# Performance work log

Hardware: AMD Instinct MI355X
Metric: run time of the kernel (lower is better)

The kernel has to match this reference:

```python
import jax, jax.numpy as jnp
import numpy as np

INF = 1e9
EPS = 1e-10
LN_EPS = 1e-5
H, CH = 8, 16  # no_heads, c_hidden


def setup_inputs() -> dict:
    key = jax.random.key(0)
    ks = jax.random.split(key, 8)
    B, S, R, C = 1, 2048, 512, 64  # batch, n_seq, n_res, c_in
    sc = 0.02
    m = jax.random.normal(ks[0], (B, S, R, C), jnp.float32)
    mask = jnp.ones((B, S, R), jnp.float32)
    ln_w = jnp.ones((C,), jnp.float32)
    ln_b = jnp.zeros((C,), jnp.float32)
    Wq = jax.random.normal(ks[1], (C, H * CH), jnp.float32) * sc
    Wk = jax.random.normal(ks[2], (C, CH), jnp.float32) * sc
    Wv = jax.random.normal(ks[3], (C, CH), jnp.float32) * sc
    Wg = jax.random.normal(ks[4], (C, H * CH), jnp.float32) * sc
    bg = jnp.ones((H * CH,), jnp.float32)  # gating init: bias = 1
    Wo = jax.random.normal(ks[5], (H * CH, C), jnp.float32) * sc
    bo = jnp.zeros((C,), jnp.float32)
    return {"m": m, "mask": mask, "ln_w": ln_w, "ln_b": ln_b, "Wq": Wq,
            "Wk": Wk, "Wv": Wv, "Wg": Wg, "bg": bg, "Wo": Wo, "bo": bo}


def reference(m, mask, ln_w, ln_b, Wq, Wk, Wv, Wg, bg, Wo, bo):
    # m: [B, S, R, C], mask: [B, S, R]
    m = jnp.swapaxes(m, -2, -3)        # [B, R, S, C] -- attend over seq per column
    mask = jnp.swapaxes(mask, -1, -2)  # [B, R, S]
    # LayerNorm over c_in
    mu = jnp.mean(m, axis=-1, keepdims=True)
    var = jnp.var(m, axis=-1, keepdims=True)
    mn = (m - mu) / jnp.sqrt(var + LN_EPS) * ln_w + ln_b  # [B, R, S, C]
    # masked mean-pooled query over seq dim
    q = jnp.sum(mn * mask[..., None], axis=-2) / (jnp.sum(mask, axis=-1)[..., None] + EPS)  # [B, R, C]
    q = (q @ Wq) * (CH ** -0.5)
    q = q.reshape(*q.shape[:-1], H, CH)  # [B, R, H, CH]
    k = mn @ Wk  # [B, R, S, CH]  (single shared K/V head)
    v = mn @ Wv  # [B, R, S, CH]
    a = jnp.einsum('brhc,brsc->brhs', q, k)
    a = a + (INF * (mask - 1.0))[..., None, :]  # additive mask bias
    a = jax.nn.softmax(a, axis=-1)               # [B, R, H, S]
    o = jnp.einsum('brhs,brsc->brhc', a, v)      # [B, R, H, CH]
    g = jax.nn.sigmoid(mn @ Wg + bg)             # [B, R, S, H*CH]
    g = g.reshape(*g.shape[:-1], H, CH)          # [B, R, S, H, CH]
    o = o[..., None, :, :] * g                   # broadcast pooled attn over seq
    o = o.reshape(*o.shape[:-2], -1)             # [B, R, S, H*CH]
    out = o @ Wo + bo                            # [B, R, S, C]
    return jnp.swapaxes(out, -2, -3)             # [B, S, R, C]
```

## Files before the change

### kernel.cpp

```cpp
#include <hip/hip_runtime.h>
#include <stdint.h>

#define S_ 2048
#define R_ 512
#define C_ 64

typedef unsigned short u16;
typedef __attribute__((ext_vector_type(8))) short bf8_t;
typedef __attribute__((ext_vector_type(4))) float f4_t;

__device__ __forceinline__ u16 f2b(float f) {
    union { float f; unsigned int i; } x; x.f = f;
    unsigned int r = x.i + 0x7fffu + ((x.i >> 16) & 1u);
    return (u16)(r >> 16);
}
__device__ __forceinline__ unsigned int pack2(float a, float b) {
    return (unsigned int)f2b(a) | ((unsigned int)f2b(b) << 16);
}
__device__ __forceinline__ void u4_to_f8(uint4 p, float* f) {
    union { unsigned int i; float f; } x;
    x.i = p.x << 16;         f[0] = x.f;
    x.i = p.x & 0xffff0000u; f[1] = x.f;
    x.i = p.y << 16;         f[2] = x.f;
    x.i = p.y & 0xffff0000u; f[3] = x.f;
    x.i = p.z << 16;         f[4] = x.f;
    x.i = p.z & 0xffff0000u; f[5] = x.f;
    x.i = p.w << 16;         f[6] = x.f;
    x.i = p.w & 0xffff0000u; f[7] = x.f;
}

__global__ __launch_bounds__(256) void k0(
    const float* __restrict__ Wk, const float* __restrict__ Wv,
    const float* __restrict__ Wg, const float* __restrict__ Wo,
    u16* __restrict__ kvT, u16* __restrict__ WgT, u16* __restrict__ WoT)
{
    int i = blockIdx.x * 256 + threadIdx.x;
    if (i < 2048) {
        int j = i >> 6, c = i & 63;
        float w = (j < 16) ? Wk[c * 16 + j] : Wv[c * 16 + (j - 16)];
        kvT[i] = f2b(w);
    }
    {
        int hc = i >> 6, c = i & 63;
        WgT[i] = f2b(Wg[c * 128 + hc]);
    }
    {
        int c = i >> 7, hc = i & 127;
        WoT[i] = f2b(Wo[hc * 64 + c]);
    }
}

__global__ __launch_bounds__(256) void k1a(
    const float* __restrict__ m, const float* __restrict__ mask,
    const float* __restrict__ lnw_g, const float* __restrict__ lnb_g,
    const u16* __restrict__ kvT_g,
    u16* __restrict__ kbuf, u16* __restrict__ vbuf,
    float* __restrict__ qsum, float* __restrict__ msum,
    u16* __restrict__ mns_g)
{
    __shared__ __attribute__((aligned(16))) u16 mns[32 * 72];
    __shared__ __attribute__((aligned(16))) u16 kva[32 * 40];
    __shared__ float qred[4][64];
    __shared__ float msred[4];

    const int tid = threadIdx.x;
    const int bi  = blockIdx.x;
    const int r   = bi >> 6;
    const int s0  = (bi & 63) << 5;
    const int wv = tid >> 6, lane = tid & 63;
    const int r16 = lane & 15, quad = lane >> 4;
    const int mt = wv & 1, nt = wv >> 1;

    bf8_t b0 = *(const bf8_t*)&kvT_g[(nt * 16 + r16) * 64 + quad * 8];
    bf8_t b1 = *(const bf8_t*)&kvT_g[(nt * 16 + r16) * 64 + 32 + quad * 8];

    const int g = tid >> 4, l = tid & 15;
    const float4 lw4 = *(const float4*)&lnw_g[4 * l];
    const float4 lb4 = *(const float4*)&lnb_g[4 * l];

    float4 qacc = {0.f, 0.f, 0.f, 0.f};
    float msacc = 0.f;
    #pragma unroll
    for (int tt = 0; tt < 2; ++tt) {
        int t = g + tt * 16;
        int s = s0 + t;
        size_t base = ((size_t)s * R_ + r) * C_;
        float4 x = *(const float4*)&m[base + 4 * l];
        float sum = x.x + x.y + x.z + x.w;
        float ssq = x.x * x.x + x.y * x.y + x.z * x.z + x.w * x.w;
        #pragma unroll
        for (int off = 1; off <= 8; off <<= 1) {
            sum += __shfl_xor(sum, off);
            ssq += __shfl_xor(ssq, off);
        }
        float mu  = sum * (1.f / 64.f);
        float var = ssq * (1.f / 64.f) - mu * mu;
        float rs  = rsqrtf(var + 1e-5f);
        float4 mn;
        mn.x = (x.x - mu) * rs * lw4.x + lb4.x;
        mn.y = (x.y - mu) * rs * lw4.y + lb4.y;
        mn.z = (x.z - mu) * rs * lw4.z + lb4.z;
        mn.w = (x.w - mu) * rs * lw4.w + lb4.w;
        float mk = mask[(size_t)s * R_ + r];
        qacc.x += mn.x * mk; qacc.y += mn.y * mk;
        qacc.z += mn.z * mk; qacc.w += mn.w * mk;
        if (l == 0) msacc += mk;
        uint2 p; p.x = pack2(mn.x, mn.y); p.y = pack2(mn.z, mn.w);
        *(uint2*)&mns[t * 72 + 4 * l] = p;
        if (mns_g)
            *(uint2*)&mns_g[((size_t)r * S_ + s) * C_ + 4 * l] = p;
    }
    qacc.x += __shfl_xor(qacc.x, 16); qacc.y += __shfl_xor(qacc.y, 16);
    qacc.z += __shfl_xor(qacc.z, 16); qacc.w += __shfl_xor(qacc.w, 16);
    qacc.x += __shfl_xor(qacc.x, 32); qacc.y += __shfl_xor(qacc.y, 32);
    qacc.z += __shfl_xor(qacc.z, 32); qacc.w += __shfl_xor(qacc.w, 32);
    msacc += __shfl_xor(msacc, 16);  msacc += __shfl_xor(msacc, 32);
    if (lane < 16) *(float4*)&qred[wv][4 * lane] = qacc;
    if (lane == 0) msred[wv] = msacc;
    __syncthreads();

    {
        f4_t acc = {0.f, 0.f, 0.f, 0.f};
        bf8_t a0 = *(const bf8_t*)&mns[(mt * 16 + r16) * 72 + quad * 8];
        bf8_t a1 = *(const bf8_t*)&mns[(mt * 16 + r16) * 72 + 32 + quad * 8];
        acc = __builtin_amdgcn_mfma_f32_16x16x32_bf16(a0, b0, acc, 0, 0, 0);
        acc = __builtin_amdgcn_mfma_f32_16x16x32_bf16(a1, b1, acc, 0, 0, 0);
        #pragma unroll
        for (int i = 0; i < 4; ++i) {
            int row = mt * 16 + quad * 4 + i;
            kva[row * 40 + nt * 16 + r16] = f2b(acc[i]);
        }
    }
    __syncthreads();

    for (int uidx = tid; uidx < 512; uidx += 256) {
        int t = uidx >> 4, u = uidx & 15;
        unsigned int val = *(const unsigned int*)&kva[t * 40 + u * 2];
        int s = s0 + t;
        size_t tb = ((size_t)r * S_ + s) * 16;
        if (u < 8) *(unsigned int*)&kbuf[tb + u * 2] = val;
        else       *(unsigned int*)&vbuf[tb + (u - 8) * 2] = val;
    }
    if (tid < 64) {
        float tot = qred[0][tid] + qred[1][tid] + qred[2][tid] + qred[3][tid];
        atomicAdd(&qsum[r * 64 + tid], tot);
    }
    if (tid == 0) atomicAdd(&msum[r], msred[0] + msred[1] + msred[2] + msred[3]);
}

__global__ __launch_bounds__(256) void k1b(
    const float* __restrict__ qsum, const float* __restrict__ msum,
    const float* __restrict__ Wq, const float* __restrict__ mask,
    const u16* __restrict__ kbuf, const u16* __restrict__ vbuf,
    float* __restrict__ opool)
{
    __shared__ float qbar[64];
    __shared__ float qh[128];
    const int tid = threadIdx.x;
    const int r   = blockIdx.x;

    if (tid < 64) qbar[tid] = qsum[r * 64 + tid] / (msum[r] + 1e-10f);
    __syncthreads();
    if (tid < 128) {
        float a = 0.f;
        #pragma unroll 8
        for (int c = 0; c < 64; ++c) a += qbar[c] * Wq[c * 128 + tid];
        qh[tid] = a * 0.25f;
    }
    __syncthreads();

    const int wv = tid >> 6, lane = tid & 63;
    const int h0 = wv, h1 = wv + 4;
    float qa[16], qb[16];
    #pragma unroll
    for (int ch = 0; ch < 16; ++ch) { qa[ch] = qh[h0 * 16 + ch]; qb[ch] = qh[h1 * 16 + ch]; }

    float m0 = -1e30f, m1 = -1e30f;
    for (int i = 0; i < 32; ++i) {
        int s = i * 64 + lane;
        size_t tb = ((size_t)r * S_ + s) * 16;
        float kf[16];
        u4_to_f8(*(const uint4*)&kbuf[tb], kf);
        u4_to_f8(*(const uint4*)&kbuf[tb + 8], kf + 8);
        float bias = (mask[(size_t)s * R_ + r] - 1.f) * 1e9f;
        float a0 = bias, a1 = bias;
        #pragma unroll
        for (int ch = 0; ch < 16; ++ch) { a0 += qa[ch] * kf[ch]; a1 += qb[ch] * kf[ch]; }
        m0 = fmaxf(m0, a0); m1 = fmaxf(m1, a1);
    }
    #pragma unroll
    for (int off = 1; off < 64; off <<= 1) {
        m0 = fmaxf(m0, __shfl_xor(m0, off));
        m1 = fmaxf(m1, __shfl_xor(m1, off));
    }
    float l0 = 0.f, l1 = 0.f;
    float o0[16], o1[16];
    #pragma unroll
    for (int ch = 0; ch < 16; ++ch) { o0[ch] = 0.f; o1[ch] = 0.f; }
    for (int i = 0; i < 32; ++i) {
        int s = i * 64 + lane;
        size_t tb = ((size_t)r * S_ + s) * 16;
        float kf[16], vf[16];
        u4_to_f8(*(const uint4*)&kbuf[tb], kf);
        u4_to_f8(*(const uint4*)&kbuf[tb + 8], kf + 8);
        u4_to_f8(*(const uint4*)&vbuf[tb], vf);
        u4_to_f8(*(const uint4*)&vbuf[tb + 8], vf + 8);
        float bias = (mask[(size_t)s * R_ + r] - 1.f) * 1e9f;
        float a0 = bias, a1 = bias;
        #pragma unroll
        for (int ch = 0; ch < 16; ++ch) { a0 += qa[ch] * kf[ch]; a1 += qb[ch] * kf[ch]; }
        float w0 = expf(a0 - m0), w1 = expf(a1 - m1);
        l0 += w0; l1 += w1;
        #pragma unroll
        for (int ch = 0; ch < 16; ++ch) { o0[ch] += w0 * vf[ch]; o1[ch] += w1 * vf[ch]; }
    }
    #pragma unroll
    for (int off = 1; off < 64; off <<= 1) {
        l0 += __shfl_xor(l0, off); l1 += __shfl_xor(l1, off);
        #pragma unroll
        for (int ch = 0; ch < 16; ++ch) {
            o0[ch] += __shfl_xor(o0[ch], off);
            o1[ch] += __shfl_xor(o1[ch], off);
        }
    }
    if (lane == 0) {
        float inv0 = 1.f / l0, inv1 = 1.f / l1;
        #pragma unroll
        for (int ch = 0; ch < 16; ++ch) {
            opool[r * 128 + h0 * 16 + ch] = o0[ch] * inv0;
            opool[r * 128 + h1 * 16 + ch] = o1[ch] * inv1;
        }
    }
}

__global__ __launch_bounds__(256) void k2m(
    const u16* __restrict__ mns_g,
    const u16* __restrict__ WgT_g, const u16* __restrict__ WoT_g,
    const float* __restrict__ bg, const float* __restrict__ bo,
    const float* __restrict__ opool, float* __restrict__ out)
{
    __shared__ __attribute__((aligned(16))) u16 olds[32 * 136];
    __shared__ __attribute__((aligned(16))) float outs[32 * 68];
    __shared__ float opl[128], bgl[128];
    __shared__ float bol[64];

    const int tid = threadIdx.x;
    const int bi  = blockIdx.x;
    const int r   = bi >> 6;
    const int s0  = (bi & 63) << 5;
    const int wv = tid >> 6, lane = tid & 63;
    const int r16 = lane & 15, quad = lane >> 4;

    const int mt  = wv >> 1;
    const int nb2 = (wv & 1) * 4;
    const int nb3 = (wv & 1) * 2;

    bf8_t wg[4][2], wo[2][4];
    #pragma unroll
    for (int i = 0; i < 4; ++i)
        #pragma unroll
        for (int kt = 0; kt < 2; ++kt)
            wg[i][kt] = *(const bf8_t*)&WgT_g[((nb2 + i) * 16 + r16) * 64 + kt * 32 + quad * 8];
    #pragma unroll
    for (int i = 0; i < 2; ++i)
        #pragma unroll
        for (int kt = 0; kt < 4; ++kt)
            wo[i][kt] = *(const bf8_t*)&WoT_g[((nb3 + i) * 16 + r16) * 128 + kt * 32 + quad * 8];

    size_t abase = ((size_t)r * S_ + s0 + mt * 16 + r16) * C_;
    bf8_t a0 = *(const bf8_t*)&mns_g[abase + quad * 8];
    bf8_t a1 = *(const bf8_t*)&mns_g[abase + 32 + quad * 8];

    if (tid < 128) { opl[tid] = opool[r * 128 + tid]; bgl[tid] = bg[tid]; }
    if (tid < 64)  { bol[tid] = bo[tid]; }
    __syncthreads();

    #pragma unroll
    for (int i = 0; i < 4; ++i) {
        f4_t acc = {0.f, 0.f, 0.f, 0.f};
        acc = __builtin_amdgcn_mfma_f32_16x16x32_bf16(a0, wg[i][0], acc, 0, 0, 0);
        acc = __builtin_amdgcn_mfma_f32_16x16x32_bf16(a1, wg[i][1], acc, 0, 0, 0);
        int hc = (nb2 + i) * 16 + r16;
        float og = opl[hc], bgv = bgl[hc];
        #pragma unroll
        for (int ii = 0; ii < 4; ++ii) {
            int row = mt * 16 + quad * 4 + ii;
            float z  = acc[ii] + bgv;
            float gv = 1.f / (1.f + expf(-z));
            olds[row * 136 + hc] = f2b(og * gv);
        }
    }
    __syncthreads();

    #pragma unroll
    for (int i = 0; i < 2; ++i) {
        f4_t acc = {0.f, 0.f, 0.f, 0.f};
        #pragma unroll
        for (int kt = 0; kt < 4; ++kt) {
            bf8_t a = *(const bf8_t*)&olds[(mt * 16 + r16) * 136 + kt * 32 + quad * 8];
            acc = __builtin_amdgcn_mfma_f32_16x16x32_bf16(a, wo[i][kt], acc, 0, 0, 0);
        }
        int c = (nb3 + i) * 16 + r16;
        float bov = bol[c];
        #pragma unroll
        for (int ii = 0; ii < 4; ++ii) {
            int row = mt * 16 + quad * 4 + ii;
            outs[row * 68 + c] = acc[ii] + bov;
        }
    }
    __syncthreads();

    const int g = tid >> 4, l = tid & 15;
    #pragma unroll
    for (int tt = 0; tt < 2; ++tt) {
        int t = g + tt * 16;
        int s = s0 + t;
        size_t base = ((size_t)s * R_ + r) * C_;
        *(float4*)&out[base + 4 * l] = *(const float4*)&outs[t * 68 + 4 * l];
    }
}

__global__ __launch_bounds__(256) void k2f(
    const float* __restrict__ m,
    const float* __restrict__ lnw_g, const float* __restrict__ lnb_g,
    const u16* __restrict__ WgT_g, const u16* __restrict__ WoT_g,
    const float* __restrict__ bg, const float* __restrict__ bo,
    const float* __restrict__ opool, float* __restrict__ out)
{
    __shared__ __attribute__((aligned(16))) u16 mns[32 * 72];
    __shared__ __attribute__((aligned(16))) u16 olds[32 * 136];
    __shared__ __attribute__((aligned(16))) float outs[32 * 68];
    __shared__ float opl[128], bgl[128];
    __shared__ float bol[64];

    const int tid = threadIdx.x;
    const int bi  = blockIdx.x;
    const int r   = bi >> 6;
    const int s0  = (bi & 63) << 5;
    const int wv = tid >> 6, lane = tid & 63;
    const int r16 = lane & 15, quad = lane >> 4;
    const int mt  = wv >> 1;
    const int nb2 = (wv & 1) * 4;
    const int nb3 = (wv & 1) * 2;

    bf8_t wg[4][2], wo[2][4];
    #pragma unroll
    for (int i = 0; i < 4; ++i)
        #pragma unroll
        for (int kt = 0; kt < 2; ++kt)
            wg[i][kt] = *(const bf8_t*)&WgT_g[((nb2 + i) * 16 + r16) * 64 + kt * 32 + quad * 8];
    #pragma unroll
    for (int i = 0; i < 2; ++i)
        #pragma unroll
        for (int kt = 0; kt < 4; ++kt)
            wo[i][kt] = *(const bf8_t*)&WoT_g[((nb3 + i) * 16 + r16) * 128 + kt * 32 + quad * 8];

    if (tid < 128) { opl[tid] = opool[r * 128 + tid]; bgl[tid] = bg[tid]; }
    if (tid < 64)  { bol[tid] = bo[tid]; }

    const int g = tid >> 4, l = tid & 15;
    const float4 lw4 = *(const float4*)&lnw_g[4 * l];
    const float4 lb4 = *(const float4*)&lnb_g[4 * l];
    #pragma unroll
    for (int tt = 0; tt < 2; ++tt) {
        int t = g + tt * 16;
        int s = s0 + t;
        size_t base = ((size_t)s * R_ + r) * C_;
        float4 x = *(const float4*)&m[base + 4 * l];
        float sum = x.x + x.y + x.z + x.w;
        float ssq = x.x * x.x + x.y * x.y + x.z * x.z + x.w * x.w;
        #pragma unroll
        for (int off = 1; off <= 8; off <<= 1) {
            sum += __shfl_xor(sum, off);
            ssq += __shfl_xor(ssq, off);
        }
        float mu  = sum * (1.f / 64.f);
        float var = ssq * (1.f / 64.f) - mu * mu;
        float rs  = rsqrtf(var + 1e-5f);
        uint2 p;
        p.x = pack2((x.x - mu) * rs * lw4.x + lb4.x, (x.y - mu) * rs * lw4.y + lb4.y);
        p.y = pack2((x.z - mu) * rs * lw4.z + lb4.z, (x.w - mu) * rs * lw4.w + lb4.w);
        *(uint2*)&mns[t * 72 + 4 * l] = p;
    }
    __syncthreads();

    #pragma unroll
    for (int i = 0; i < 4; ++i) {
        f4_t acc = {0.f, 0.f, 0.f, 0.f};
        #pragma unroll
        for (int kt = 0; kt < 2; ++kt) {
            bf8_t a = *(const bf8_t*)&mns[(mt * 16 + r16) * 72 + kt * 32 + quad * 8];
            acc = __builtin_amdgcn_mfma_f32_16x16x32_bf16(a, wg[i][kt], acc, 0, 0, 0);
        }
        int hc = (nb2 + i) * 16 + r16;
        float og = opl[hc], bgv = bgl[hc];
        #pragma unroll
        for (int ii = 0; ii < 4; ++ii) {
            int row = mt * 16 + quad * 4 + ii;
            float z  = acc[ii] + bgv;
            float gv = 1.f / (1.f + expf(-z));
            olds[row * 136 + hc] = f2b(og * gv);
        }
    }
    __syncthreads();

    #pragma unroll
    for (int i = 0; i < 2; ++i) {
        f4_t acc = {0.f, 0.f, 0.f, 0.f};
        #pragma unroll
        for (int kt = 0; kt < 4; ++kt) {
            bf8_t a = *(const bf8_t*)&olds[(mt * 16 + r16) * 136 + kt * 32 + quad * 8];
            acc = __builtin_amdgcn_mfma_f32_16x16x32_bf16(a, wo[i][kt], acc, 0, 0, 0);
        }
        int c = (nb3 + i) * 16 + r16;
        float bov = bol[c];
        #pragma unroll
        for (int ii = 0; ii < 4; ++ii) {
            int row = mt * 16 + quad * 4 + ii;
            outs[row * 68 + c] = acc[ii] + bov;
        }
    }
    __syncthreads();

    #pragma unroll
    for (int tt = 0; tt < 2; ++tt) {
        int t = g + tt * 16;
        int s = s0 + t;
        size_t base = ((size_t)s * R_ + r) * C_;
        *(float4*)&out[base + 4 * l] = *(const float4*)&outs[t * 68 + 4 * l];
    }
}

extern "C" void kernel_launch(void* const* d_in, const int* in_sizes, int n_in,
                              void* d_out, int out_size, void* d_ws, size_t ws_size,
                              hipStream_t stream)
{
    const float* m    = (const float*)d_in[0];
    const float* mask = (const float*)d_in[1];
    const float* lnw  = (const float*)d_in[2];
    const float* lnb  = (const float*)d_in[3];
    const float* Wq   = (const float*)d_in[4];
    const float* Wk   = (const float*)d_in[5];
    const float* Wv   = (const float*)d_in[6];
    const float* Wg   = (const float*)d_in[7];
    const float* bg   = (const float*)d_in[8];
    const float* Wo   = (const float*)d_in[9];
    const float* bo   = (const float*)d_in[10];
    float* out = (float*)d_out;

    char* ws = (char*)d_ws;
    u16*   kbuf  = (u16*)ws;
    u16*   vbuf  = (u16*)(ws + 33554432ull);
    float* qsum  = (float*)(ws + 67108864ull);
    float* msum  = (float*)(ws + 67239936ull);
    float* opool = (float*)(ws + 67241984ull);
    u16*   kvT   = (u16*)(ws + 67504128ull);
    u16*   WgT   = (u16*)(ws + 67508224ull);
    u16*   WoT   = (u16*)(ws + 67524608ull);
    u16*   mns_g = (u16*)(ws + 67540992ull);
    const size_t WS_NEED_MNS = 67540992ull + 134217728ull;
    const bool use_mns = ws_size >= WS_NEED_MNS;

    hipMemsetAsync(ws + 67108864ull, 0, 131072 + 2048, stream);
    k0<<<32, 256, 0, stream>>>(Wk, Wv, Wg, Wo, kvT, WgT, WoT);
    k1a<<<32768, 256, 0, stream>>>(m, mask, lnw, lnb, kvT, kbuf, vbuf, qsum, msum,
                                   use_mns ? mns_g : (u16*)nullptr);
    k1b<<<512, 256, 0, stream>>>(qsum, msum, Wq, mask, kbuf, vbuf, opool);
    if (use_mns)
        k2m<<<32768, 256, 0, stream>>>(mns_g, WgT, WoT, bg, bo, opool, out);
    else
        k2f<<<32768, 256, 0, stream>>>(m, lnw, lnb, WgT, WoT, bg, bo, opool, out);
}
```

Baseline: 849.2 us.

## Split pooled attention over sequence chunks with a separate combine kernel

The per-column attention kernel, which previously used 512 blocks each looping over all 2048 sequence positions, is split into 4096 blocks that each handle a 256-position chunk. Each block writes its partial max, sum and weighted V to a workspace buffer, and a small combine kernel merges the eight chunks per column with a log-sum-exp rescale. This is meant to fill the GPU better during that phase. Separately, expf and the division in the sigmoid gate are replaced with the fast __expf and rcp intrinsics, trading a little accuracy for cheaper transcendentals. The chunked path runs only when the workspace is large enough, and it adds a kernel launch and an extra round trip through global memory for the partial results.

```diff
diff --git a/kernel.cpp b/kernel.cpp
--- a/kernel.cpp
+++ b/kernel.cpp
@@ -148,7 +148,120 @@
     if (tid == 0) atomicAdd(&msum[r], msred[0] + msred[1] + msred[2] + msred[3]);
 }
 
-__global__ __launch_bounds__(256) void k1b(
+__global__ __launch_bounds__(256) void k1bp(
+    const float* __restrict__ qsum, const float* __restrict__ msum,
+    const float* __restrict__ Wq, const float* __restrict__ mask,
+    const u16* __restrict__ kbuf, const u16* __restrict__ vbuf,
+    float* __restrict__ pbuf)
+{
+    __shared__ float qbar[64];
+    __shared__ float qh[128];
+    const int tid = threadIdx.x;
+    const int bi  = blockIdx.x;
+    const int r   = bi >> 3;
+    const int ck  = bi & 7;
+
+    if (tid < 64) qbar[tid] = qsum[r * 64 + tid] / (msum[r] + 1e-10f);
+    __syncthreads();
+    if (tid < 128) {
+        float a = 0.f;
+        #pragma unroll 8
+        for (int c = 0; c < 64; ++c) a += qbar[c] * Wq[c * 128 + tid];
+        qh[tid] = a * 0.25f;
+    }
+    __syncthreads();
+
+    const int wv = tid >> 6, lane = tid & 63;
+    const int h0 = wv, h1 = wv + 4;
+    float qa[16], qb[16];
+    #pragma unroll
+    for (int ch = 0; ch < 16; ++ch) { qa[ch] = qh[h0 * 16 + ch]; qb[ch] = qh[h1 * 16 + ch]; }
+
+    const int sbase = ck * 256;
+    float m0 = -1e30f, m1 = -1e30f;
+    #pragma unroll
+    for (int i = 0; i < 4; ++i) {
+        int s = sbase + i * 64 + lane;
+        size_t tb = ((size_t)r * S_ + s) * 16;
+        float kf[16];
+        u4_to_f8(*(const uint4*)&kbuf[tb], kf);
+        u4_to_f8(*(const uint4*)&kbuf[tb + 8], kf + 8);
+        float bias = (mask[(size_t)s * R_ + r] - 1.f) * 1e9f;
+        float a0 = bias, a1 = bias;
+        #pragma unroll
+        for (int ch = 0; ch < 16; ++ch) { a0 += qa[ch] * kf[ch]; a1 += qb[ch] * kf[ch]; }
+        m0 = fmaxf(m0, a0); m1 = fmaxf(m1, a1);
+    }
+    #pragma unroll
+    for (int off = 1; off < 64; off <<= 1) {
+        m0 = fmaxf(m0, __shfl_xor(m0, off));
+        m1 = fmaxf(m1, __shfl_xor(m1, off));
+    }
+    float l0 = 0.f, l1 = 0.f;
+    float o0[16], o1[16];
+    #pragma unroll
+    for (int ch = 0; ch < 16; ++ch) { o0[ch] = 0.f; o1[ch] = 0.f; }
+    #pragma unroll
+    for (int i = 0; i < 4; ++i) {
+        int s = sbase + i * 64 + lane;
+        size_t tb = ((size_t)r * S_ + s) * 16;
+        float kf[16], vf[16];
+        u4_to_f8(*(const uint4*)&kbuf[tb], kf);
+        u4_to_f8(*(const uint4*)&kbuf[tb + 8], kf + 8);
+        u4_to_f8(*(const uint4*)&vbuf[tb], vf);
+        u4_to_f8(*(const uint4*)&vbuf[tb + 8], vf + 8);
+        float bias = (mask[(size_t)s * R_ + r] - 1.f) * 1e9f;
+        float a0 = bias, a1 = bias;
+        #pragma unroll
+        for (int ch = 0; ch < 16; ++ch) { a0 += qa[ch] * kf[ch]; a1 += qb[ch] * kf[ch]; }
+        float w0 = __expf(a0 - m0), w1 = __expf(a1 - m1);
+        l0 += w0; l1 += w1;
+        #pragma unroll
+        for (int ch = 0; ch < 16; ++ch) { o0[ch] += w0 * vf[ch]; o1[ch] += w1 * vf[ch]; }
+    }
+    #pragma unroll
+    for (int off = 1; off < 64; off <<= 1) {
+        l0 += __shfl_xor(l0, off); l1 += __shfl_xor(l1, off);
+        #pragma unroll
+        for (int ch = 0; ch < 16; ++ch) {
+            o0[ch] += __shfl_xor(o0[ch], off);
+            o1[ch] += __shfl_xor(o1[ch], off);
+        }
+    }
+    if (lane == 0) {
+        size_t p0 = (((size_t)r * 8 + h0) * 8 + ck) * 18;
+        size_t p1 = (((size_t)r * 8 + h1) * 8 + ck) * 18;
+        pbuf[p0] = m0; pbuf[p0 + 1] = l0;
+        pbuf[p1] = m1; pbuf[p1 + 1] = l1;
+        #pragma unroll
+        for (int ch = 0; ch < 16; ++ch) {
+            pbuf[p0 + 2 + ch] = o0[ch];
+            pbuf[p1 + 2 + ch] = o1[ch];
+        }
+    }
+}
+
+__global__ __launch_bounds__(128) void k1c(
+    const float* __restrict__ pbuf, float* __restrict__ opool)
+{
+    const int r = blockIdx.x;
+    const int tid = threadIdx.x;
+    const int h = tid >> 4, ch = tid & 15;
+    size_t base = (((size_t)r * 8 + h) * 8) * 18;
+    float M = -1e30f;
+    #pragma unroll
+    for (int i = 0; i < 8; ++i) M = fmaxf(M, pbuf[base + i * 18]);
+    float L = 0.f, O = 0.f;
+    #pragma unroll
+    for (int i = 0; i < 8; ++i) {
+        float sc = __expf(pbuf[base + i * 18] - M);
+        L += pbuf[base + i * 18 + 1] * sc;
+        O += pbuf[base + i * 18 + 2 + ch] * sc;
+    }
+    opool[r * 128 + tid] = O / L;
+}
+
+__global__ __launch_bounds__(256) void k1b_mono(
     const float* __restrict__ qsum, const float* __restrict__ msum,
     const float* __restrict__ Wq, const float* __restrict__ mask,
     const u16* __restrict__ kbuf, const u16* __restrict__ vbuf,
@@ -209,7 +322,7 @@
         float a0 = bias, a1 = bias;
         #pragma unroll
         for (int ch = 0; ch < 16; ++ch) { a0 += qa[ch] * kf[ch]; a1 += qb[ch] * kf[ch]; }
-        float w0 = expf(a0 - m0), w1 = expf(a1 - m1);
+        float w0 = __expf(a0 - m0), w1 = __expf(a1 - m1);
         l0 += w0; l1 += w1;
         #pragma unroll
         for (int ch = 0; ch < 16; ++ch) { o0[ch] += w0 * vf[ch]; o1[ch] += w1 * vf[ch]; }
@@ -286,7 +399,7 @@
         for (int ii = 0; ii < 4; ++ii) {
             int row = mt * 16 + quad * 4 + ii;
             float z  = acc[ii] + bgv;
-            float gv = 1.f / (1.f + expf(-z));
+            float gv = __builtin_amdgcn_rcpf(1.f + __expf(-z));
             olds[row * 136 + hc] = f2b(og * gv);
         }
     }
@@ -398,7 +511,7 @@
         for (int ii = 0; ii < 4; ++ii) {
             int row = mt * 16 + quad * 4 + ii;
             float z  = acc[ii] + bgv;
-            float gv = 1.f / (1.f + expf(-z));
+            float gv = __builtin_amdgcn_rcpf(1.f + __expf(-z));
             olds[row * 136 + hc] = f2b(og * gv);
         }
     }
@@ -458,14 +571,22 @@
     u16*   WgT   = (u16*)(ws + 67508224ull);
     u16*   WoT   = (u16*)(ws + 67524608ull);
     u16*   mns_g = (u16*)(ws + 67540992ull);
-    const size_t WS_NEED_MNS = 67540992ull + 134217728ull;
-    const bool use_mns = ws_size >= WS_NEED_MNS;
+    float* pbuf  = (float*)(ws + 201758720ull);
+    const size_t NEED_MNS = 67540992ull + 134217728ull;
+    const size_t NEED_PB  = 201758720ull + 2359296ull;
+    const bool use_mns = ws_size >= NEED_MNS;
+    const bool use_pb  = ws_size >= NEED_PB;
 
     hipMemsetAsync(ws + 67108864ull, 0, 131072 + 2048, stream);
     k0<<<32, 256, 0, stream>>>(Wk, Wv, Wg, Wo, kvT, WgT, WoT);
     k1a<<<32768, 256, 0, stream>>>(m, mask, lnw, lnb, kvT, kbuf, vbuf, qsum, msum,
                                    use_mns ? mns_g : (u16*)nullptr);
-    k1b<<<512, 256, 0, stream>>>(qsum, msum, Wq, mask, kbuf, vbuf, opool);
+    if (use_pb) {
+        k1bp<<<4096, 256, 0, stream>>>(qsum, msum, Wq, mask, kbuf, vbuf, pbuf);
+        k1c<<<512, 128, 0, stream>>>(pbuf, opool);
+    } else {
+        k1b_mono<<<512, 256, 0, stream>>>(qsum, msum, Wq, mask, kbuf, vbuf, opool);
+    }
     if (use_mns)
         k2m<<<32768, 256, 0, stream>>>(mns_g, WgT, WoT, bg, bo, opool, out);
     else
```

Result: faster. 827.3 us (-2.6%).
